# Kernel tuning notes

Measured on AMD Instinct MI355X. Metric: run time of the kernel, lower is better.

## Reference

```python
import jax, jax.numpy as jnp
import numpy as np
import math

B, T, D_MODEL, N_HEAD = 2, 2048, 1024, 16
NUM_BUCKETS, MAX_DIST = 32, 128
D_HEAD = D_MODEL // N_HEAD


def _relative_position_bucket(rel_pos, num_buckets=NUM_BUCKETS, max_distance=MAX_DIST):
    # bidirectional=True branch of the torch code
    nb = num_buckets // 2
    buckets = (rel_pos > 0).astype(jnp.int32) * nb
    rel_pos = jnp.abs(rel_pos)
    max_exact = nb // 2
    is_small = rel_pos < max_exact
    # guard log(0); masked out by is_small anyway
    large = max_exact + (
        jnp.log(jnp.maximum(rel_pos, 1).astype(jnp.float32) / max_exact)
        / math.log(max_distance / max_exact) * (nb - max_exact)
    ).astype(jnp.int32)
    large = jnp.minimum(large, nb - 1)
    return buckets + jnp.where(is_small, rel_pos, large)


def compute_bias(rel_bias, q_len, kv_len):
    qp = jnp.arange(q_len, dtype=jnp.int32)[:, None]
    kp = jnp.arange(kv_len, dtype=jnp.int32)[None, :]
    buckets = _relative_position_bucket(kp - qp)          # [Tq, Tkv]
    vals = rel_bias[buckets]                              # [Tq, Tkv, H]
    return jnp.transpose(vals, (2, 0, 1))                 # [H, Tq, Tkv]


def setup_inputs() -> dict:
    key = jax.random.key(0)
    ks = jax.random.split(key, 9)
    inp = {
        'q': jax.random.normal(ks[0], (B, T, D_MODEL), jnp.float32),
        'k': jax.random.normal(ks[1], (B, T, D_MODEL), jnp.float32),
        'v': jax.random.normal(ks[2], (B, T, D_MODEL), jnp.float32),
        'mask': jax.random.randint(ks[3], (B, T, T), 0, 2, jnp.int32),
        'Wq': jax.random.normal(ks[4], (D_MODEL, D_MODEL), jnp.float32) * 0.02,
        'Wk': jax.random.normal(ks[5], (D_MODEL, D_MODEL), jnp.float32) * 0.02,
        'Wv': jax.random.normal(ks[6], (D_MODEL, D_MODEL), jnp.float32) * 0.02,
        'Wfc': jax.random.normal(ks[7], (D_MODEL, D_MODEL), jnp.float32) * 0.02,
        'rel_bias': jax.random.normal(ks[8], (NUM_BUCKETS, N_HEAD), jnp.float32) * 0.02,
    }
    return inp


def reference(q, k, v, mask, Wq, Wk, Wv, Wfc, rel_bias):
    b, tq, _ = q.shape
    tkv = k.shape[1]
    qh = (q @ Wq).reshape(b, tq, N_HEAD, D_HEAD)
    kh = (k @ Wk).reshape(b, tkv, N_HEAD, D_HEAD)
    vh = (v @ Wv).reshape(b, tkv, N_HEAD, D_HEAD)
    attn = jnp.einsum('blhd,bthd->bhlt', qh, kh) / np.sqrt(D_HEAD).astype(np.float32)
    position_bias = compute_bias(rel_bias, tq, tkv)       # [H, Tq, Tkv]
    attn = attn + position_bias[None]                     # broadcast over batch
    attn = jnp.where(mask[:, None] == 0, -1e9, attn)
    attn = jax.nn.softmax(attn, axis=-1)                  # dropout: eval mode (identity)
    out = jnp.einsum('bhlt,bthd->blhd', attn, vh).reshape(b, tq, D_MODEL)
    out = out @ Wfc
    return out, position_bias[:, None]                    # bias returned as [H,1,Tq,Tkv] like torch
```

## Files before the change

### kernel.cpp

```cpp
#include <hip/hip_runtime.h>
#include <math.h>

#define TT 2048
#define BB 2
#define HH 16
#define DMODEL 1024
#define NREL 4095

typedef __attribute__((ext_vector_type(8)))  _Float16 half8;
typedef __attribute__((ext_vector_type(4)))  _Float16 half4;
typedef __attribute__((ext_vector_type(16))) float    f32x16;
typedef __attribute__((ext_vector_type(4)))  int      int4v;

#define EXP2F(x) __builtin_amdgcn_exp2f(x)

__device__ __forceinline__ f32x16 zero16() {
    f32x16 v;
#pragma unroll
    for (int i = 0; i < 16; ++i) v[i] = 0.f;
    return v;
}

__device__ __forceinline__ unsigned pkh(float a, float b) {
    union { _Float16 h[2]; unsigned u; } x;
    x.h[0] = (_Float16)a; x.h[1] = (_Float16)b;
    return x.u;
}

__device__ __forceinline__ void gload16(const void* g, void* l) {
    __builtin_amdgcn_global_load_lds(
        (const __attribute__((address_space(1))) void*)g,
        (__attribute__((address_space(3))) void*)l, 16, 0, 0);
}

__device__ __forceinline__ int rel_bucket(int rel) {
    int base = rel > 0 ? 16 : 0;
    int r = rel < 0 ? -rel : rel;
    int lb;
    if (r < 8)       lb = r;
    else if (r < 12) lb = 8;
    else if (r < 16) lb = 9;
    else if (r < 23) lb = 10;
    else if (r < 32) lb = 11;
    else if (r < 46) lb = 12;
    else if (r < 64) lb = 13;
    else if (r < 91) lb = 14;
    else             lb = 15;
    return base + lb;
}

__global__ __launch_bounds__(256) void prep_kernel(
    const float* __restrict__ q, const float* __restrict__ k,
    const float* __restrict__ v, const int* __restrict__ mask,
    const float* __restrict__ W0, const float* __restrict__ W1,
    const float* __restrict__ W2, const float* __restrict__ W3,
    const float* __restrict__ rel_bias,
    _Float16* __restrict__ q16, _Float16* __restrict__ k16,
    _Float16* __restrict__ v16, _Float16* __restrict__ WT,
    float* __restrict__ btable, unsigned* __restrict__ mb)
{
    __shared__ float t[64][65];
    int bid = blockIdx.x, tid = threadIdx.x;
    if (bid < 256) {
        int idx = bid * 256 + tid;
        if (idx < HH * NREL) {
            int h = idx / NREL, ri = idx % NREL;
            btable[idx] = rel_bias[rel_bucket(ri - (TT - 1)) * HH + h];
        }
    } else if (bid < 1280) {
        int zz = (bid - 256) >> 8, inner = (bid - 256) & 255;
        const float* src = zz == 0 ? W0 : zz == 1 ? W1 : zz == 2 ? W2 : W3;
        _Float16* dst = WT + (size_t)zz * DMODEL * DMODEL;
        int k0 = (inner >> 4) * 64, n0 = (inner & 15) * 64;
        int r = tid >> 4, c4 = (tid & 15) * 4;
#pragma unroll
        for (int i = 0; i < 4; ++i) {
            float4 vv = *(const float4*)(src + (size_t)(k0 + r + 16 * i) * DMODEL + n0 + c4);
            t[r + 16 * i][c4] = vv.x; t[r + 16 * i][c4 + 1] = vv.y;
            t[r + 16 * i][c4 + 2] = vv.z; t[r + 16 * i][c4 + 3] = vv.w;
        }
        __syncthreads();
        int rn = tid >> 2, ck = (tid & 3) * 16;
        half8 h0, h1;
#pragma unroll
        for (int j = 0; j < 8; ++j) h0[j] = (_Float16)t[ck + j][rn];
#pragma unroll
        for (int j = 0; j < 8; ++j) h1[j] = (_Float16)t[ck + 8 + j][rn];
        *(half8*)(dst + (size_t)(n0 + rn) * DMODEL + k0 + ck) = h0;
        *(half8*)(dst + (size_t)(n0 + rn) * DMODEL + k0 + ck + 8) = h1;
    } else if (bid < 7424) {
        int zz = (bid - 1280) >> 11, inner = (bid - 1280) & 2047;
        const float* src = zz == 0 ? q : zz == 1 ? k : v;
        _Float16* dst = zz == 0 ? q16 : zz == 1 ? k16 : v16;
        int i = inner * 256 + tid;
        const float4* in4 = (const float4*)src;
        float4 v0 = in4[(size_t)i * 2], v1 = in4[(size_t)i * 2 + 1];
        half8 h = {(_Float16)v0.x, (_Float16)v0.y, (_Float16)v0.z, (_Float16)v0.w,
                   (_Float16)v1.x, (_Float16)v1.y, (_Float16)v1.z, (_Float16)v1.w};
        *(half8*)(dst + (size_t)i * 8) = h;
    } else {
        int g = (bid - 7424) * 256 + tid;
        int vv = mask[g];
        unsigned long long bal = __ballot(vv != 0);
        if ((g & 63) == 0) {
            int word = g >> 5;
            mb[word]     = (unsigned)bal;
            mb[word + 1] = (unsigned)(bal >> 32);
        }
    }
}

__global__ __launch_bounds__(256) void gemm_proj3(
    const _Float16* __restrict__ q16, const _Float16* __restrict__ k16,
    const _Float16* __restrict__ v16, const _Float16* __restrict__ WT,
    _Float16* __restrict__ qhf, _Float16* __restrict__ khf,
    _Float16* __restrict__ vtf, int zbase)
{
    __shared__ __align__(16) char lds[65536];
    int z = zbase + blockIdx.z;
    const _Float16* A  = z == 0 ? q16 : z == 1 ? k16 : v16;
    const _Float16* Bt = WT + (size_t)z * DMODEL * DMODEL;
    int bm = blockIdx.x * 128, bn = blockIdx.y * 128;
    int tid = threadIdx.x;
    int wv = tid >> 6, lane = tid & 63, hi = lane >> 5;
    int lo = lane & 31;
    int wr = wv >> 1, wc = wv & 1;
    int srow = wv * 32 + (lane >> 3);
    int scol = (lane & 7) * 8;
    const _Float16* Abase = A  + (size_t)(bm + srow) * DMODEL + scol;
    const _Float16* Bbase = Bt + (size_t)(bn + srow) * DMODEL + scol;

    f32x16 acc[2][2];
    acc[0][0] = zero16(); acc[0][1] = zero16();
    acc[1][0] = zero16(); acc[1][1] = zero16();

    auto stage = [&](int buf, int kt) {
#pragma unroll
        for (int t = 0; t < 4; ++t) {
            gload16(Abase + (size_t)t * 8 * DMODEL + kt * 64, lds + buf + wv * 4096 + t * 1024);
            gload16(Bbase + (size_t)t * 8 * DMODEL + kt * 64, lds + buf + 16384 + wv * 4096 + t * 1024);
        }
    };
    auto compute = [&](int buf) {
#pragma unroll
        for (int kk = 0; kk < 4; ++kk) {
            int cs = 2 * kk + hi;
            half8 a[2], b[2];
#pragma unroll
            for (int i = 0; i < 2; ++i) {
                a[i] = *(const half8*)(lds + buf + (wr * 64 + i * 32 + lo) * 128 + cs * 16);
                b[i] = *(const half8*)(lds + buf + 16384 + (wc * 64 + i * 32 + lo) * 128 + cs * 16);
            }
            acc[0][0] = __builtin_amdgcn_mfma_f32_32x32x16_f16(a[0], b[0], acc[0][0], 0, 0, 0);
            acc[0][1] = __builtin_amdgcn_mfma_f32_32x32x16_f16(a[0], b[1], acc[0][1], 0, 0, 0);
            acc[1][0] = __builtin_amdgcn_mfma_f32_32x32x16_f16(a[1], b[0], acc[1][0], 0, 0, 0);
            acc[1][1] = __builtin_amdgcn_mfma_f32_32x32x16_f16(a[1], b[1], acc[1][1], 0, 0, 0);
        }
    };

    stage(0, 0);
    __syncthreads();
    for (int kt = 0; kt < 16; kt += 2) {
        stage(32768, kt + 1);
        compute(0);
        __syncthreads();
        stage(0, kt + 2 < 16 ? kt + 2 : 15);
        compute(32768);
        __syncthreads();
    }

    if (z < 2) {
        _Float16* C = z == 0 ? qhf : khf;
#pragma unroll
        for (int j = 0; j < 2; ++j) {
            int n = bn + wc * 64 + j * 32 + lo;
            int h = n >> 6, d = n & 63;
#pragma unroll
            for (int i = 0; i < 2; ++i) {
                int mb2 = bm + wr * 64 + i * 32 + 4 * hi;
#pragma unroll
                for (int r = 0; r < 16; ++r) {
                    int m = mb2 + (r & 3) + 8 * (r >> 2);
                    int b = m >> 11, t = m & (TT - 1);
                    C[((size_t)(b * HH + h) * TT + t) * 64 + d] = (_Float16)acc[i][j][r];
                }
            }
        }
    } else {
#pragma unroll
        for (int j = 0; j < 2; ++j) {
            int n = bn + wc * 64 + j * 32 + lo;
            int h = n >> 6, d = n & 63;
#pragma unroll
            for (int i = 0; i < 2; ++i) {
                int mb2 = bm + wr * 64 + i * 32 + 4 * hi;
                int b = mb2 >> 11, tb = mb2 & (TT - 1);
#pragma unroll
                for (int r4 = 0; r4 < 4; ++r4) {
                    half4 hv = {(_Float16)acc[i][j][4 * r4 + 0], (_Float16)acc[i][j][4 * r4 + 1],
                                (_Float16)acc[i][j][4 * r4 + 2], (_Float16)acc[i][j][4 * r4 + 3]};
                    *(half4*)(vtf + ((size_t)(b * HH + h) * 64 + d) * TT + tb + 8 * r4) = hv;
                }
            }
        }
    }
}

__global__ __launch_bounds__(256) void attn_bias_kernel(
    const _Float16* __restrict__ qh, const _Float16* __restrict__ kh,
    const _Float16* __restrict__ vt, const unsigned* __restrict__ maskbits,
    const float* __restrict__ btable, _Float16* __restrict__ Oout,
    float* __restrict__ out1)
{
    __shared__ float bias_lds[4096];
    int bid = blockIdx.x;
    int tid = threadIdx.x;
    if (bid >= 512) {
        const int n4 = HH * TT * TT / 4, stride = 2048 * 256;
        for (int i4 = (bid - 512) * 256 + tid; i4 < n4; i4 += stride) {
            int i = i4 * 4;
            int kk = i & (TT - 1);
            int qq = (i >> 11) & (TT - 1);
            int hh2 = i >> 22;
            const float* btp = btable + hh2 * NREL + (kk - qq + (TT - 1));
            float4 vv = make_float4(btp[0], btp[1], btp[2], btp[3]);
            reinterpret_cast<float4*>(out1)[i4] = vv;
        }
        return;
    }

    int xcd = bid & 7, j = bid >> 3;
    int qt = j & 15, bh = xcd + 8 * (j >> 4);
    int h = bh & 15, b = bh >> 4;
    int wv = tid >> 6, lane = tid & 63, lo = lane & 31, hi = lane >> 5;
    int q0 = qt * 128 + wv * 32;

    {
        const float* bsrc = btable + h * NREL;
#pragma unroll
        for (int i = 0; i < 16; ++i) {
            int idx = i * 256 + tid;
            bias_lds[idx] = bsrc[idx < NREL ? idx : NREL - 1] * 1.44269504f;
        }
    }

    const size_t bhoff = (size_t)(b * HH + h);
    const _Float16* Q = qh + (bhoff * TT + q0) * 64;
    const _Float16* K = kh + bhoff * TT * 64;
    const _Float16* V = vt + bhoff * 64 * TT;

    half8 qf[4];
#pragma unroll
    for (int c = 0; c < 4; ++c)
        qf[c] = *(const half8*)(Q + (size_t)lo * 64 + c * 16 + hi * 8);

    const int bofs = (TT - 1) - (q0 + lo) + 4 * hi;
    const unsigned* mw = maskbits + ((size_t)b * TT + q0 + lo) * 64;
    const float SC = 0.125f * 1.44269504f;

    f32x16 acco0 = zero16(), acco1 = zero16();
    float m = -INFINITY, l = 0.f;

    __syncthreads();

    for (int kt = 0; kt < 16; ++kt) {
        int k0 = kt * 128;
        unsigned wmA0 = mw[4 * kt], wmA1 = mw[4 * kt + 1];
        unsigned wmB0 = mw[4 * kt + 2], wmB1 = mw[4 * kt + 3];

        f32x16 sA0 = zero16(), sA1 = zero16(), sB0 = zero16(), sB1 = zero16();
        {
            half8 kf[4];
#pragma unroll
            for (int c = 0; c < 4; ++c)
                kf[c] = *(const half8*)(K + (size_t)(k0 + lo) * 64 + c * 16 + hi * 8);
            __builtin_amdgcn_s_setprio(1);
#pragma unroll
            for (int c = 0; c < 4; ++c)
                sA0 = __builtin_amdgcn_mfma_f32_32x32x16_f16(kf[c], qf[c], sA0, 0, 0, 0);
            __builtin_amdgcn_s_setprio(0);
#pragma unroll
            for (int c = 0; c < 4; ++c)
                kf[c] = *(const half8*)(K + (size_t)(k0 + 32 + lo) * 64 + c * 16 + hi * 8);
            __builtin_amdgcn_s_setprio(1);
#pragma unroll
            for (int c = 0; c < 4; ++c)
                sA1 = __builtin_amdgcn_mfma_f32_32x32x16_f16(kf[c], qf[c], sA1, 0, 0, 0);
            __builtin_amdgcn_s_setprio(0);
#pragma unroll
            for (int c = 0; c < 4; ++c)
                kf[c] = *(const half8*)(K + (size_t)(k0 + 64 + lo) * 64 + c * 16 + hi * 8);
            __builtin_amdgcn_s_setprio(1);
#pragma unroll
            for (int c = 0; c < 4; ++c)
                sB0 = __builtin_amdgcn_mfma_f32_32x32x16_f16(kf[c], qf[c], sB0, 0, 0, 0);
            __builtin_amdgcn_s_setprio(0);
#pragma unroll
            for (int c = 0; c < 4; ++c)
                kf[c] = *(const half8*)(K + (size_t)(k0 + 96 + lo) * 64 + c * 16 + hi * 8);
            __builtin_amdgcn_s_setprio(1);
#pragma unroll
            for (int c = 0; c < 4; ++c)
                sB1 = __builtin_amdgcn_mfma_f32_32x32x16_f16(kf[c], qf[c], sB1, 0, 0, 0);
            __builtin_amdgcn_s_setprio(0);
        }

        unsigned wsA0 = wmA0 >> (hi * 4), wsA1 = wmA1 >> (hi * 4);
        unsigned wsB0 = wmB0 >> (hi * 4), wsB1 = wmB1 >> (hi * 4);
        int bbase = bofs + k0;
#pragma unroll
        for (int r = 0; r < 16; ++r) {
            int sh = (r & 3) + 8 * (r >> 2);
            float a0 = fmaf(sA0[r], SC, bias_lds[bbase + sh]);
            float a1 = fmaf(sA1[r], SC, bias_lds[bbase + sh + 32]);
            float b0 = fmaf(sB0[r], SC, bias_lds[bbase + sh + 64]);
            float b1 = fmaf(sB1[r], SC, bias_lds[bbase + sh + 96]);
            sA0[r] = ((wsA0 >> sh) & 1) ? a0 : -1e9f;
            sA1[r] = ((wsA1 >> sh) & 1) ? a1 : -1e9f;
            sB0[r] = ((wsB0 >> sh) & 1) ? b0 : -1e9f;
            sB1[r] = ((wsB1 >> sh) & 1) ? b1 : -1e9f;
        }

        float tr[8];
#pragma unroll
        for (int r = 0; r < 8; ++r) {
            float x0 = fmaxf(fmaxf(sA0[r], sA0[r + 8]), fmaxf(sA1[r], sA1[r + 8]));
            float x1 = fmaxf(fmaxf(sB0[r], sB0[r + 8]), fmaxf(sB1[r], sB1[r + 8]));
            tr[r] = fmaxf(x0, x1);
        }
#pragma unroll
        for (int r = 0; r < 4; ++r) tr[r] = fmaxf(tr[r], tr[r + 4]);
        float tm = fmaxf(fmaxf(tr[0], tr[1]), fmaxf(tr[2], tr[3]));
        tm = fmaxf(tm, __shfl_xor(tm, 32));
        float mnew = fmaxf(m, tm);
        float corr = EXP2F(m - mnew);
        m = mnew;

#pragma unroll
        for (int r = 0; r < 16; ++r) sA0[r] = EXP2F(sA0[r] - m);
#pragma unroll
        for (int r = 0; r < 16; ++r) sA1[r] = EXP2F(sA1[r] - m);
#pragma unroll
        for (int r = 0; r < 16; ++r) sB0[r] = EXP2F(sB0[r] - m);
#pragma unroll
        for (int r = 0; r < 16; ++r) sB1[r] = EXP2F(sB1[r] - m);
#pragma unroll
        for (int r = 0; r < 8; ++r)
            tr[r] = ((sA0[r] + sA0[r + 8]) + (sA1[r] + sA1[r + 8]))
                  + ((sB0[r] + sB0[r + 8]) + (sB1[r] + sB1[r + 8]));
#pragma unroll
        for (int r = 0; r < 4; ++r) tr[r] += tr[r + 4];
        float rs = (tr[0] + tr[1]) + (tr[2] + tr[3]);
        rs += __shfl_xor(rs, 32);
        l = l * corr + rs;
#pragma unroll
        for (int r = 0; r < 16; ++r) { acco0[r] *= corr; acco1[r] *= corr; }

        half8 pbA[4], pbB[4];
#pragma unroll
        for (int g = 0; g < 2; ++g)
#pragma unroll
            for (int hc = 0; hc < 2; ++hc) {
                int r0 = hc * 8;
                float p0 = g ? sA1[r0 + 0] : sA0[r0 + 0];
                float p1 = g ? sA1[r0 + 1] : sA0[r0 + 1];
                float p2 = g ? sA1[r0 + 2] : sA0[r0 + 2];
                float p3 = g ? sA1[r0 + 3] : sA0[r0 + 3];
                float p4 = g ? sA1[r0 + 4] : sA0[r0 + 4];
                float p5 = g ? sA1[r0 + 5] : sA0[r0 + 5];
                float p6 = g ? sA1[r0 + 6] : sA0[r0 + 6];
                float p7 = g ? sA1[r0 + 7] : sA0[r0 + 7];
                unsigned w0 = pkh(p0, p1);
                unsigned w2 = pkh(p4, p5);
                asm("v_permlane32_swap_b32 %0, %1" : "+v"(w0), "+v"(w2));
                unsigned w1 = pkh(p2, p3);
                unsigned w3 = pkh(p6, p7);
                asm("v_permlane32_swap_b32 %0, %1" : "+v"(w1), "+v"(w3));
                union { int4v i; half8 hf; } cv;
                cv.i = (int4v){(int)w0, (int)w1, (int)w2, (int)w3};
                pbA[2 * g + hc] = cv.hf;
            }
#pragma unroll
        for (int g = 0; g < 2; ++g)
#pragma unroll
            for (int hc = 0; hc < 2; ++hc) {
                int r0 = hc * 8;
                float p0 = g ? sB1[r0 + 0] : sB0[r0 + 0];
                float p1 = g ? sB1[r0 + 1] : sB0[r0 + 1];
                float p2 = g ? sB1[r0 + 2] : sB0[r0 + 2];
                float p3 = g ? sB1[r0 + 3] : sB0[r0 + 3];
                float p4 = g ? sB1[r0 + 4] : sB0[r0 + 4];
                float p5 = g ? sB1[r0 + 5] : sB0[r0 + 5];
                float p6 = g ? sB1[r0 + 6] : sB0[r0 + 6];
                float p7 = g ? sB1[r0 + 7] : sB0[r0 + 7];
                unsigned w0 = pkh(p0, p1);
                unsigned w2 = pkh(p4, p5);
                asm("v_permlane32_swap_b32 %0, %1" : "+v"(w0), "+v"(w2));
                unsigned w1 = pkh(p2, p3);
                unsigned w3 = pkh(p6, p7);
                asm("v_permlane32_swap_b32 %0, %1" : "+v"(w1), "+v"(w3));
                union { int4v i; half8 hf; } cv;
                cv.i = (int4v){(int)w0, (int)w1, (int)w2, (int)w3};
                pbB[2 * g + hc] = cv.hf;
            }

        {
            half8 vf[4];
#pragma unroll
            for (int c = 0; c < 4; ++c)
                vf[c] = *(const half8*)(V + (size_t)lo * TT + k0 + c * 16 + hi * 8);
            __builtin_amdgcn_s_setprio(1);
#pragma unroll
            for (int c = 0; c < 4; ++c)
                acco0 = __builtin_amdgcn_mfma_f32_32x32x16_f16(vf[c], pbA[c], acco0, 0, 0, 0);
            __builtin_amdgcn_s_setprio(0);
#pragma unroll
            for (int c = 0; c < 4; ++c)
                vf[c] = *(const half8*)(V + (size_t)lo * TT + k0 + 64 + c * 16 + hi * 8);
            __builtin_amdgcn_s_setprio(1);
#pragma unroll
            for (int c = 0; c < 4; ++c)
                acco0 = __builtin_amdgcn_mfma_f32_32x32x16_f16(vf[c], pbB[c], acco0, 0, 0, 0);
            __builtin_amdgcn_s_setprio(0);
#pragma unroll
            for (int c = 0; c < 4; ++c)
                vf[c] = *(const half8*)(V + (size_t)(32 + lo) * TT + k0 + c * 16 + hi * 8);
            __builtin_amdgcn_s_setprio(1);
#pragma unroll
            for (int c = 0; c < 4; ++c)
                acco1 = __builtin_amdgcn_mfma_f32_32x32x16_f16(vf[c], pbA[c], acco1, 0, 0, 0);
            __builtin_amdgcn_s_setprio(0);
#pragma unroll
            for (int c = 0; c < 4; ++c)
                vf[c] = *(const half8*)(V + (size_t)(32 + lo) * TT + k0 + 64 + c * 16 + hi * 8);
            __builtin_amdgcn_s_setprio(1);
#pragma unroll
            for (int c = 0; c < 4; ++c)
                acco1 = __builtin_amdgcn_mfma_f32_32x32x16_f16(vf[c], pbB[c], acco1, 0, 0, 0);
            __builtin_amdgcn_s_setprio(0);
        }
    }

    float inv = 1.f / l;
    _Float16* op = Oout + (bhoff * TT + q0 + lo) * 64;
#pragma unroll
    for (int r4 = 0; r4 < 4; ++r4) {
        int d0 = 8 * r4 + 4 * hi;
        half4 h0 = {(_Float16)(acco0[4 * r4 + 0] * inv), (_Float16)(acco0[4 * r4 + 1] * inv),
                    (_Float16)(acco0[4 * r4 + 2] * inv), (_Float16)(acco0[4 * r4 + 3] * inv)};
        *(half4*)(op + d0) = h0;
        half4 h1 = {(_Float16)(acco1[4 * r4 + 0] * inv), (_Float16)(acco1[4 * r4 + 1] * inv),
                    (_Float16)(acco1[4 * r4 + 2] * inv), (_Float16)(acco1[4 * r4 + 3] * inv)};
        *(half4*)(op + d0 + 32) = h1;
    }
}

__global__ __launch_bounds__(256) void fc_kernel(
    const _Float16* __restrict__ O, const _Float16* __restrict__ Bt,
    float* __restrict__ out0)
{
    __shared__ __align__(16) char lds[65536];
    int bid = blockIdx.x, tid = threadIdx.x;
    int bm = (bid & 31) * 128, bn = (bid >> 5) * 128;
    int wv = tid >> 6, lane = tid & 63, lo = lane & 31, hi = lane >> 5;
    int wr = wv >> 1, wc = wv & 1;
    int srow = wv * 32 + (lane >> 3);
    int scol = (lane & 7) * 8;
    int bb = bm >> 11, tbase = bm & (TT - 1);
    const _Float16* Abase = O + ((size_t)(bb * HH) * TT + tbase + srow) * 64 + scol;
    const _Float16* Bbase = Bt + (size_t)(bn + srow) * DMODEL + scol;

    f32x16 acc[2][2];
    acc[0][0] = zero16(); acc[0][1] = zero16();
    acc[1][0] = zero16(); acc[1][1] = zero16();

    auto stage = [&](int buf, int kt) {
#pragma unroll
        for (int t = 0; t < 4; ++t) {
            gload16(Abase + (size_t)kt * TT * 64 + (size_t)t * 8 * 64, lds + buf + wv * 4096 + t * 1024);
            gload16(Bbase + (size_t)t * 8 * DMODEL + kt * 64, lds + buf + 16384 + wv * 4096 + t * 1024);
        }
    };
    auto compute = [&](int buf) {
#pragma unroll
        for (int kk = 0; kk < 4; ++kk) {
            int cs = 2 * kk + hi;
            half8 a[2], b[2];
#pragma unroll
            for (int i = 0; i < 2; ++i) {
                a[i] = *(const half8*)(lds + buf + (wr * 64 + i * 32 + lo) * 128 + cs * 16);
                b[i] = *(const half8*)(lds + buf + 16384 + (wc * 64 + i * 32 + lo) * 128 + cs * 16);
            }
            acc[0][0] = __builtin_amdgcn_mfma_f32_32x32x16_f16(a[0], b[0], acc[0][0], 0, 0, 0);
            acc[0][1] = __builtin_amdgcn_mfma_f32_32x32x16_f16(a[0], b[1], acc[0][1], 0, 0, 0);
            acc[1][0] = __builtin_amdgcn_mfma_f32_32x32x16_f16(a[1], b[0], acc[1][0], 0, 0, 0);
            acc[1][1] = __builtin_amdgcn_mfma_f32_32x32x16_f16(a[1], b[1], acc[1][1], 0, 0, 0);
        }
    };

    stage(0, 0);
    __syncthreads();
    for (int kt = 0; kt < 16; kt += 2) {
        stage(32768, kt + 1);
        compute(0);
        __syncthreads();
        stage(0, kt + 2 < 16 ? kt + 2 : 15);
        compute(32768);
        __syncthreads();
    }

#pragma unroll
    for (int j = 0; j < 2; ++j) {
        int n = bn + wc * 64 + j * 32 + lo;
#pragma unroll
        for (int i = 0; i < 2; ++i) {
            int mb2 = bm + wr * 64 + i * 32 + 4 * hi;
#pragma unroll
            for (int r = 0; r < 16; ++r) {
                int m = mb2 + (r & 3) + 8 * (r >> 2);
                out0[(size_t)m * DMODEL + n] = acc[i][j][r];
            }
        }
    }
}

extern "C" void kernel_launch(void* const* d_in, const int* in_sizes, int n_in,
                              void* d_out, int out_size, void* d_ws, size_t ws_size,
                              hipStream_t stream) {
    const float* q        = (const float*)d_in[0];
    const float* k        = (const float*)d_in[1];
    const float* v        = (const float*)d_in[2];
    const int*   mask     = (const int*)  d_in[3];
    const float* Wq       = (const float*)d_in[4];
    const float* Wk       = (const float*)d_in[5];
    const float* Wv       = (const float*)d_in[6];
    const float* Wfc      = (const float*)d_in[7];
    const float* rel_bias = (const float*)d_in[8];

    float* out0 = (float*)d_out;
    float* out1 = out0 + (size_t)BB * TT * DMODEL;

    char* w = (char*)d_ws;
    _Float16* q16 = (_Float16*)(w);
    _Float16* k16 = (_Float16*)(w + ((size_t)8  << 20));
    _Float16* v16 = (_Float16*)(w + ((size_t)16 << 20));
    _Float16* qhf = (_Float16*)(w + ((size_t)24 << 20));
    _Float16* khf = (_Float16*)(w + ((size_t)32 << 20));
    _Float16* WT  = (_Float16*)(w + ((size_t)40 << 20));
    float*    btable = (float*)(w + ((size_t)48 << 20));
    unsigned* mbits  = (unsigned*)(w + ((size_t)48 << 20) + ((size_t)1 << 19));
    bool big = ws_size >= ((size_t)58 << 20);
    _Float16* vtf = big ? (_Float16*)(w + ((size_t)49 << 20) + ((size_t)1 << 19))
                        : k16;
    _Float16* O = v16;

    prep_kernel<<<dim3(40192), dim3(256), 0, stream>>>(
        q, k, v, mask, Wq, Wk, Wv, Wfc, rel_bias, q16, k16, v16, WT, btable, mbits);

    if (big) {
        gemm_proj3<<<dim3(32, 8, 3), dim3(256), 0, stream>>>(q16, k16, v16, WT,
                                                             qhf, khf, vtf, 0);
    } else {
        gemm_proj3<<<dim3(32, 8, 1), dim3(256), 0, stream>>>(q16, k16, v16, WT, qhf, khf, vtf, 0);
        gemm_proj3<<<dim3(32, 8, 1), dim3(256), 0, stream>>>(q16, k16, v16, WT, qhf, khf, vtf, 1);
        gemm_proj3<<<dim3(32, 8, 1), dim3(256), 0, stream>>>(q16, k16, v16, WT, qhf, khf, vtf, 2);
    }

    attn_bias_kernel<<<dim3(512 + 2048), dim3(256), 0, stream>>>(
        qhf, khf, vtf, mbits, btable, O, out1);

    fc_kernel<<<dim3(256), dim3(256), 0, stream>>>(
        O, WT + (size_t)3 * DMODEL * DMODEL, out0);
}
```

Measured before the change: 289.2 us.

## Move position-bias output writes from attention kernel into projection GEMM launch

The 256 MB position-bias broadcast write moves out of the attention kernel and into extra blocks of the QKV projection GEMM launch, which now uses a flat 1D grid. The attention kernel launches only its 512 compute blocks. The aim is to overlap the bandwidth-bound bias store with the compute-bound GEMM instead of the attention MFMA work, and to free the attention kernel from competing for memory bandwidth. The risk is that the GEMM blocks now contend with the heavy store traffic, and the bias block count changes from 2048 to 1024.

```diff
diff --git a/kernel.cpp b/kernel.cpp
--- a/kernel.cpp
+++ b/kernel.cpp
@@ -114,14 +114,30 @@
     const _Float16* __restrict__ q16, const _Float16* __restrict__ k16,
     const _Float16* __restrict__ v16, const _Float16* __restrict__ WT,
     _Float16* __restrict__ qhf, _Float16* __restrict__ khf,
-    _Float16* __restrict__ vtf, int zbase)
+    _Float16* __restrict__ vtf, const float* __restrict__ btable,
+    float* __restrict__ out1, int zbase, int ngemm)
 {
     __shared__ __align__(16) char lds[65536];
-    int z = zbase + blockIdx.z;
+    int bid = blockIdx.x, tid = threadIdx.x;
+    if (bid >= ngemm * 256) {
+        const int n4 = HH * TT * TT / 4;
+        int nbias = gridDim.x - ngemm * 256;
+        int stride = nbias * 256;
+        for (int i4 = (bid - ngemm * 256) * 256 + tid; i4 < n4; i4 += stride) {
+            int i = i4 * 4;
+            int kk = i & (TT - 1);
+            int qq = (i >> 11) & (TT - 1);
+            int hh2 = i >> 22;
+            const float* btp = btable + hh2 * NREL + (kk - qq + (TT - 1));
+            float4 vv = make_float4(btp[0], btp[1], btp[2], btp[3]);
+            reinterpret_cast<float4*>(out1)[i4] = vv;
+        }
+        return;
+    }
+    int z = zbase + (bid >> 8);
     const _Float16* A  = z == 0 ? q16 : z == 1 ? k16 : v16;
     const _Float16* Bt = WT + (size_t)z * DMODEL * DMODEL;
-    int bm = blockIdx.x * 128, bn = blockIdx.y * 128;
-    int tid = threadIdx.x;
+    int bm = (bid & 31) * 128, bn = ((bid >> 5) & 7) * 128;
     int wv = tid >> 6, lane = tid & 63, hi = lane >> 5;
     int lo = lane & 31;
     int wr = wv >> 1, wc = wv & 1;
@@ -206,32 +222,17 @@
     }
 }
 
-__global__ __launch_bounds__(256) void attn_bias_kernel(
+__global__ __launch_bounds__(256) void attn_mfma(
     const _Float16* __restrict__ qh, const _Float16* __restrict__ kh,
     const _Float16* __restrict__ vt, const unsigned* __restrict__ maskbits,
-    const float* __restrict__ btable, _Float16* __restrict__ Oout,
-    float* __restrict__ out1)
+    const float* __restrict__ btable, _Float16* __restrict__ Oout)
 {
     __shared__ float bias_lds[4096];
     int bid = blockIdx.x;
-    int tid = threadIdx.x;
-    if (bid >= 512) {
-        const int n4 = HH * TT * TT / 4, stride = 2048 * 256;
-        for (int i4 = (bid - 512) * 256 + tid; i4 < n4; i4 += stride) {
-            int i = i4 * 4;
-            int kk = i & (TT - 1);
-            int qq = (i >> 11) & (TT - 1);
-            int hh2 = i >> 22;
-            const float* btp = btable + hh2 * NREL + (kk - qq + (TT - 1));
-            float4 vv = make_float4(btp[0], btp[1], btp[2], btp[3]);
-            reinterpret_cast<float4*>(out1)[i4] = vv;
-        }
-        return;
-    }
-
     int xcd = bid & 7, j = bid >> 3;
     int qt = j & 15, bh = xcd + 8 * (j >> 4);
     int h = bh & 15, b = bh >> 4;
+    int tid = threadIdx.x;
     int wv = tid >> 6, lane = tid & 63, lo = lane & 31, hi = lane >> 5;
     int q0 = qt * 128 + wv * 32;
 
@@ -558,16 +559,19 @@
         q, k, v, mask, Wq, Wk, Wv, Wfc, rel_bias, q16, k16, v16, WT, btable, mbits);
 
     if (big) {
-        gemm_proj3<<<dim3(32, 8, 3), dim3(256), 0, stream>>>(q16, k16, v16, WT,
-                                                             qhf, khf, vtf, 0);
+        gemm_proj3<<<dim3(768 + 1024), dim3(256), 0, stream>>>(
+            q16, k16, v16, WT, qhf, khf, vtf, btable, out1, 0, 3);
     } else {
-        gemm_proj3<<<dim3(32, 8, 1), dim3(256), 0, stream>>>(q16, k16, v16, WT, qhf, khf, vtf, 0);
-        gemm_proj3<<<dim3(32, 8, 1), dim3(256), 0, stream>>>(q16, k16, v16, WT, qhf, khf, vtf, 1);
-        gemm_proj3<<<dim3(32, 8, 1), dim3(256), 0, stream>>>(q16, k16, v16, WT, qhf, khf, vtf, 2);
-    }
-
-    attn_bias_kernel<<<dim3(512 + 2048), dim3(256), 0, stream>>>(
-        qhf, khf, vtf, mbits, btable, O, out1);
+        gemm_proj3<<<dim3(256), dim3(256), 0, stream>>>(
+            q16, k16, v16, WT, qhf, khf, vtf, btable, out1, 0, 1);
+        gemm_proj3<<<dim3(256), dim3(256), 0, stream>>>(
+            q16, k16, v16, WT, qhf, khf, vtf, btable, out1, 1, 1);
+        gemm_proj3<<<dim3(256 + 1024), dim3(256), 0, stream>>>(
+            q16, k16, v16, WT, qhf, khf, vtf, btable, out1, 2, 1);
+    }
+
+    attn_mfma<<<dim3(BB * HH * 16), dim3(256), 0, stream>>>(
+        qhf, khf, vtf, mbits, btable, O);
 
     fc_kernel<<<dim3(256), dim3(256), 0, stream>>>(
         O, WT + (size_t)3 * DMODEL * DMODEL, out0);
```

Measured after the change: 288.7 us. Within noise of the previous version (-0.2%).
